# Kernel tuning notes

Measured on AMD Instinct MI355X. Metric: run time of the kernel, lower is better.

The kernel has to match this reference:

```python
import jax, jax.numpy as jnp
import numpy as np

B, N, M = 2, 256, 512
IN_F, OUT_F = 256, 128
NEG_INF = -1.0e12


def setup_inputs() -> dict:
    key = jax.random.key(0)
    kx, ka, kw, kv = jax.random.split(key, 4)
    X = jax.random.normal(kx, (B, N, IN_F), dtype=jnp.float32)
    # node-edge incidence (0/1), kept float as in the torch module
    A = jax.random.randint(ka, (B, N, M), 0, 2).astype(jnp.float32)
    # xavier-uniform-ish scale: gain*sqrt(6/(fan_in+fan_out))
    w_scale = 1.414 * np.sqrt(6.0 / (IN_F + OUT_F))
    a_scale = 1.414 * np.sqrt(6.0 / (2 * OUT_F + 1))
    W = jax.random.uniform(kw, (IN_F, OUT_F), jnp.float32, -w_scale, w_scale)
    a = jax.random.uniform(kv, (2 * OUT_F, 1), jnp.float32, -a_scale, a_scale)
    return {"X": X, "A": A, "W": W, "a": a}


def reference(X, A, W, a):
    H = X @ W                                   # [B, N, F]
    F_ = H.shape[-1]
    # per-edge degree, zeros clamped to 1
    degree = jnp.sum(A, axis=1)[..., None]      # [B, M, 1]
    degree = jnp.where(degree == 0, 1.0, degree)
    Em = jnp.einsum('bnm,bnf->bmf', A, H) / degree   # [B, M, F]
    # faithful replication of torch: cat along dim=1 then view (note: NOT a
    # per-pair concat along features; rows of H and Em get interleaved)
    Hrep = jnp.tile(H, (1, 1, M)).reshape(B, N * M, F_)   # [B, N*M, F]
    EmRep = jnp.tile(Em, (1, N, 1))                        # [B, N*M, F]
    a_input = jnp.concatenate([Hrep, EmRep], axis=1).reshape(B, N, M, 2 * F_)
    e = jax.nn.leaky_relu(jnp.squeeze(a_input @ a, -1), negative_slope=0.01)  # [B, N, M]
    attention = jax.nn.softmax(jnp.where(A > 0, e, NEG_INF), axis=2)          # [B, N, M]
    h_prime = jnp.einsum('bnm,bnf->bmf', attention, H)                         # [B, M, F]
    return h_prime
```

## Files before the change

### kernel.cpp

```cpp
#include <hip/hip_runtime.h>

#define NN 256
#define MM 512
#define INF_ 256
#define OUTF 128

__global__ __launch_bounds__(256) void k_gemm(const float* __restrict__ X,
                                              const float* __restrict__ W,
                                              const float* __restrict__ avec,
                                              float* __restrict__ H,
                                              float* __restrict__ h0,
                                              float* __restrict__ h1,
                                              float* __restrict__ cH,
                                              float* __restrict__ S) {
    const int blk = blockIdx.x;
    const int t = threadIdx.x;
    const int f = t & 127, kh = t >> 7;
    const int bn0 = blk * 2, bn1 = bn0 + 1;
    __shared__ float xs[2][INF_];
    xs[0][t] = X[bn0 * INF_ + t];
    xs[1][t] = X[bn1 * INF_ + t];
    __syncthreads();
    float acc0 = 0.f, acc1 = 0.f;
    const float* Wp = W + kh * 128 * OUTF + f;
    const float* x0 = xs[0] + kh * 128;
    const float* x1 = xs[1] + kh * 128;
#pragma unroll 8
    for (int k = 0; k < 128; ++k) {
        float w = Wp[k * OUTF];
        acc0 = fmaf(x0[k], w, acc0);
        acc1 = fmaf(x1[k], w, acc1);
    }
    __shared__ float accs[2][256];
    accs[0][t] = acc0;
    accs[1][t] = acc1;
    __syncthreads();
    const int r = t >> 7, tf = t & 127;
    const int bn = bn0 + r;
    float a2 = accs[r][tf] + accs[r][tf + 128];
    H[bn * OUTF + tf] = a2;
    float p0 = a2 * avec[tf];
    float p1 = a2 * avec[OUTF + tf];
#pragma unroll
    for (int off = 32; off >= 1; off >>= 1) {
        p0 += __shfl_down(p0, off);
        p1 += __shfl_down(p1, off);
    }
    __shared__ float r0[4], r1[4];
    const int wv = t >> 6, ln = t & 63;
    if (ln == 0) { r0[wv] = p0; r1[wv] = p1; }
    __syncthreads();
    if (ln == 0 && (wv & 1) == 0) {
        float s0 = r0[wv] + r0[wv + 1];
        float s1 = r1[wv] + r1[wv + 1];
        h0[bn] = s0;
        h1[bn] = s1;
        float hA = s0 + s1;
        cH[bn] = hA > 0.f ? hA : 0.01f * hA;
        int n = bn & 255;
        if (n >= 128) S[(bn >> 8) * 128 + n - 128] = 0.f;
    }
}

__global__ __launch_bounds__(256) void k_emg(const float* __restrict__ A,
                                             const float* __restrict__ h0,
                                             const float* __restrict__ h1,
                                             const float* __restrict__ cH,
                                             float* __restrict__ g,
                                             float* __restrict__ rs0,
                                             float* __restrict__ rs1,
                                             float* __restrict__ S) {
    const int blk = blockIdx.x;
    const int t = threadIdx.x;
    if (blk < 32) {
        const int b = blk >> 4, mq = blk & 15;
        const int m_l = t & 31, n_l = t >> 5;
        __shared__ float sh0[NN], sh1[NN];
        __shared__ float sd[256], ss0[256], ss1[256];
        __shared__ float se0[32], se1[32], sg[16];
        sh0[t] = h0[b * NN + t];
        sh1[t] = h1[b * NN + t];
        __syncthreads();
        const float* Ap = A + (size_t)b * NN * MM + mq * 32 + m_l;
        float d = 0.f, s0 = 0.f, s1 = 0.f;
#pragma unroll 8
        for (int i = 0; i < 32; ++i) {
            int n = n_l * 32 + i;
            float av = Ap[n * MM];
            d += av;
            s0 += av * sh0[n];
            s1 += av * sh1[n];
        }
        sd[t] = d; ss0[t] = s0; ss1[t] = s1;
        __syncthreads();
        if (t < 32) {
            float D = 0.f, S0 = 0.f, S1 = 0.f;
#pragma unroll
            for (int j = 0; j < 8; ++j) {
                D  += sd[j * 32 + t];
                S0 += ss0[j * 32 + t];
                S1 += ss1[j * 32 + t];
            }
            if (D == 0.f) D = 1.f;
            se0[t] = S0 / D;
            se1[t] = S1 / D;
        }
        __syncthreads();
        if (t < 16) {
            float v = se0[2 * t] + se1[2 * t + 1];
            v = v > 0.f ? v : 0.01f * v;
            float gv = expf(v);
            g[b * MM + 16 * mq + t] = gv;
            g[b * MM + 256 + 16 * mq + t] = gv;
            sg[t] = gv;
        }
        __syncthreads();
        {
            const int u = t & 15, ng = t >> 4;
            const float gv = sg[u];
            const float* Alo = A + (size_t)b * NN * MM + 16 * mq + u;
#pragma unroll
            for (int step = 0; step < 8; ++step) {
                int n = 128 + ng + 16 * step;
                const float* Ar = Alo + (size_t)n * MM;
                float val = gv * (Ar[0] + Ar[256]);
                val += __shfl_xor(val, 1);
                val += __shfl_xor(val, 2);
                val += __shfl_xor(val, 4);
                val += __shfl_xor(val, 8);
                if (u == 0) atomicAdd(&S[b * 128 + n - 128], val);
            }
        }
    } else {
        const int wv = t >> 6, lane = t & 63;
        const int l = (blk - 32) * 4 + wv;
        const int b = l >> 7, n = l & 127;
        const int bn = b * NN + n;
        const float* Ar = A + (size_t)bn * MM;
        float c0 = 0.f, c1 = 0.f;
#pragma unroll
        for (int i = 0; i < 8; ++i) {
            float av = Ar[lane + 64 * i];
            if (i < 4) c0 += av; else c1 += av;
        }
#pragma unroll
        for (int off = 32; off >= 1; off >>= 1) {
            c0 += __shfl_xor(c0, off);
            c1 += __shfl_xor(c1, off);
        }
        if (lane == 0) {
            float ch0 = cH[b * NN + 2 * n];
            float ch1 = cH[b * NN + 2 * n + 1];
            float mx = fmaxf(c0 > 0.f ? ch0 : -INFINITY,
                             c1 > 0.f ? ch1 : -INFINITY);
            float e0 = c0 > 0.f ? expf(ch0 - mx) : 0.f;
            float e1 = c1 > 0.f ? expf(ch1 - mx) : 0.f;
            float inv = 1.f / (c0 * e0 + c1 * e1);
            rs0[bn] = e0 * inv;
            rs1[bn] = e1 * inv;
        }
    }
}

__global__ __launch_bounds__(256) void k_out(const float* __restrict__ A,
                                             const float* __restrict__ H,
                                             const float* __restrict__ g,
                                             const float* __restrict__ rs0,
                                             const float* __restrict__ rs1,
                                             const float* __restrict__ S,
                                             float* __restrict__ out) {
    __shared__ float sW[NN];
    __shared__ float sA[4][NN];
    __shared__ float2 sacc[2][4][64];
    const int blk = blockIdx.x;
    const int b = blk >> 7, mq = blk & 127;
    const int m_base = 4 * mq;
    const int t = threadIdx.x;
    if (t < 128) {
        sW[t] = ((mq < 64) ? rs0 : rs1)[b * NN + t];
    } else {
        sW[t] = 1.f / S[b * 128 + (t - 128)];
    }
    const float* Ac = A + (size_t)(b * NN + t) * MM + m_base;
    sA[0][t] = Ac[0];
    sA[1][t] = Ac[1];
    sA[2][t] = Ac[2];
    sA[3][t] = Ac[3];
    __syncthreads();
    const int f2 = t & 63;
    const int nh = (t >> 6) & 1;
    const int mh = t >> 7;
    const float* sA0 = sA[2 * mh];
    const float* sA1 = sA[2 * mh + 1];
    const float2* H2 = (const float2*)H + (size_t)b * NN * 64 + f2;
    float2 acc0 = {0.f, 0.f}, acc1 = {0.f, 0.f};
#pragma unroll 8
    for (int i = 0; i < 128; ++i) {
        int n = nh * 128 + i;
        float w = sW[n];
        float2 hv = H2[n * 64];
        float c0 = sA0[n] * w;
        float c1 = sA1[n] * w;
        acc0.x = fmaf(c0, hv.x, acc0.x);
        acc0.y = fmaf(c0, hv.y, acc0.y);
        acc1.x = fmaf(c1, hv.x, acc1.x);
        acc1.y = fmaf(c1, hv.y, acc1.y);
    }
    sacc[nh][2 * mh][f2] = acc0;
    sacc[nh][2 * mh + 1][f2] = acc1;
    __syncthreads();
    {
        const int ml = t >> 6, f2b = t & 63;
        const int m = m_base + ml;
        float eE = g[b * MM + m];
        float2 lo = sacc[0][ml][f2b];
        float2 hi = sacc[1][ml][f2b];
        float2 r;
        r.x = lo.x + eE * hi.x;
        r.y = lo.y + eE * hi.y;
        ((float2*)out)[((size_t)b * MM + m) * 64 + f2b] = r;
    }
}

extern "C" void kernel_launch(void* const* d_in, const int* in_sizes, int n_in,
                              void* d_out, int out_size, void* d_ws, size_t ws_size,
                              hipStream_t stream) {
    const float* X = (const float*)d_in[0];
    const float* A = (const float*)d_in[1];
    const float* W = (const float*)d_in[2];
    const float* a = (const float*)d_in[3];
    float* out = (float*)d_out;
    float* ws = (float*)d_ws;

    float* H   = ws;
    float* h0  = ws + 65536;
    float* h1  = ws + 66048;
    float* cH  = ws + 66560;
    float* g   = ws + 67072;
    float* rs0 = ws + 68096;
    float* rs1 = ws + 68608;
    float* S   = ws + 69120;

    k_gemm<<<256, 256, 0, stream>>>(X, W, a, H, h0, h1, cH, S);
    k_emg<<<96, 256, 0, stream>>>(A, h0, h1, cH, g, rs0, rs1, S);
    k_out<<<256, 256, 0, stream>>>(A, H, g, rs0, rs1, S, out);
}
```

Baseline: 24.65 us.

## Move softmax row normalization into GEMM kernel and widen per-block tiles

The per-node row count and softmax normalization (rs0/rs1), previously computed by extra blocks in the edge kernel, are now computed inside the GEMM kernel. Each GEMM block handles four nodes and also reads the matching A rows. That removes the cH round trip and shrinks the edge kernel to 32 blocks. The GEMM and output kernels now process 4 rows and 8 edges per block respectively, and the output kernel loads A with float4. This raises reuse of W and H per block but halves the grid size, which reduces parallelism on a wide GPU.

Result: slower. 29.73 us (+20.6%).

```diff
diff --git a/kernel.cpp b/kernel.cpp
--- a/kernel.cpp
+++ b/kernel.cpp
@@ -6,158 +6,174 @@
 #define OUTF 128
 
 __global__ __launch_bounds__(256) void k_gemm(const float* __restrict__ X,
+                                              const float* __restrict__ A,
                                               const float* __restrict__ W,
                                               const float* __restrict__ avec,
                                               float* __restrict__ H,
                                               float* __restrict__ h0,
                                               float* __restrict__ h1,
-                                              float* __restrict__ cH,
+                                              float* __restrict__ rs0,
+                                              float* __restrict__ rs1,
                                               float* __restrict__ S) {
     const int blk = blockIdx.x;
+    const int b = blk >> 6, q = blk & 63;
+    const int bn0 = b * NN + 4 * q;
     const int t = threadIdx.x;
     const int f = t & 127, kh = t >> 7;
-    const int bn0 = blk * 2, bn1 = bn0 + 1;
-    __shared__ float xs[2][INF_];
-    xs[0][t] = X[bn0 * INF_ + t];
-    xs[1][t] = X[bn1 * INF_ + t];
-    __syncthreads();
-    float acc0 = 0.f, acc1 = 0.f;
-    const float* Wp = W + kh * 128 * OUTF + f;
-    const float* x0 = xs[0] + kh * 128;
-    const float* x1 = xs[1] + kh * 128;
+    const int wv = t >> 6, ln = t & 63;
+
+    __shared__ float xs[4][INF_];
+    __shared__ float accs[4][256];
+    __shared__ float r0[4], r1[4];
+    __shared__ float sch[4];
+    __shared__ float scnt[4];
+
+    xs[0][t] = X[(bn0 + 0) * INF_ + t];
+    xs[1][t] = X[(bn0 + 1) * INF_ + t];
+    xs[2][t] = X[(bn0 + 2) * INF_ + t];
+    xs[3][t] = X[(bn0 + 3) * INF_ + t];
+    __syncthreads();
+
+    float acc0 = 0.f, acc1 = 0.f, acc2 = 0.f, acc3 = 0.f;
+    {
+        const float* Wp = W + kh * 128 * OUTF + f;
+        const float* x0 = xs[0] + kh * 128;
+        const float* x1 = xs[1] + kh * 128;
+        const float* x2 = xs[2] + kh * 128;
+        const float* x3 = xs[3] + kh * 128;
 #pragma unroll 8
-    for (int k = 0; k < 128; ++k) {
-        float w = Wp[k * OUTF];
-        acc0 = fmaf(x0[k], w, acc0);
-        acc1 = fmaf(x1[k], w, acc1);
-    }
-    __shared__ float accs[2][256];
+        for (int k = 0; k < 128; ++k) {
+            float w = Wp[k * OUTF];
+            acc0 = fmaf(x0[k], w, acc0);
+            acc1 = fmaf(x1[k], w, acc1);
+            acc2 = fmaf(x2[k], w, acc2);
+            acc3 = fmaf(x3[k], w, acc3);
+        }
+    }
     accs[0][t] = acc0;
     accs[1][t] = acc1;
-    __syncthreads();
-    const int r = t >> 7, tf = t & 127;
-    const int bn = bn0 + r;
-    float a2 = accs[r][tf] + accs[r][tf + 128];
-    H[bn * OUTF + tf] = a2;
-    float p0 = a2 * avec[tf];
-    float p1 = a2 * avec[OUTF + tf];
-#pragma unroll
-    for (int off = 32; off >= 1; off >>= 1) {
-        p0 += __shfl_down(p0, off);
-        p1 += __shfl_down(p1, off);
-    }
-    __shared__ float r0[4], r1[4];
-    const int wv = t >> 6, ln = t & 63;
-    if (ln == 0) { r0[wv] = p0; r1[wv] = p1; }
-    __syncthreads();
-    if (ln == 0 && (wv & 1) == 0) {
-        float s0 = r0[wv] + r0[wv + 1];
-        float s1 = r1[wv] + r1[wv + 1];
-        h0[bn] = s0;
-        h1[bn] = s1;
-        float hA = s0 + s1;
-        cH[bn] = hA > 0.f ? hA : 0.01f * hA;
-        int n = bn & 255;
-        if (n >= 128) S[(bn >> 8) * 128 + n - 128] = 0.f;
-    }
-}
-
-__global__ __launch_bounds__(256) void k_emg(const float* __restrict__ A,
-                                             const float* __restrict__ h0,
-                                             const float* __restrict__ h1,
-                                             const float* __restrict__ cH,
-                                             float* __restrict__ g,
-                                             float* __restrict__ rs0,
-                                             float* __restrict__ rs1,
-                                             float* __restrict__ S) {
-    const int blk = blockIdx.x;
-    const int t = threadIdx.x;
-    if (blk < 32) {
-        const int b = blk >> 4, mq = blk & 15;
-        const int m_l = t & 31, n_l = t >> 5;
-        __shared__ float sh0[NN], sh1[NN];
-        __shared__ float sd[256], ss0[256], ss1[256];
-        __shared__ float se0[32], se1[32], sg[16];
-        sh0[t] = h0[b * NN + t];
-        sh1[t] = h1[b * NN + t];
+    accs[2][t] = acc2;
+    accs[3][t] = acc3;
+    __syncthreads();
+
+#pragma unroll
+    for (int pass = 0; pass < 2; ++pass) {
+        const int row = 2 * pass + (t >> 7);
+        const int tf = t & 127;
+        float a2 = accs[row][tf] + accs[row][tf + 128];
+        H[(bn0 + row) * OUTF + tf] = a2;
+        float p0 = a2 * avec[tf];
+        float p1 = a2 * avec[OUTF + tf];
+#pragma unroll
+        for (int off = 32; off >= 1; off >>= 1) {
+            p0 += __shfl_down(p0, off);
+            p1 += __shfl_down(p1, off);
+        }
+        if (ln == 0) { r0[wv] = p0; r1[wv] = p1; }
         __syncthreads();
-        const float* Ap = A + (size_t)b * NN * MM + mq * 32 + m_l;
-        float d = 0.f, s0 = 0.f, s1 = 0.f;
-#pragma unroll 8
-        for (int i = 0; i < 32; ++i) {
-            int n = n_l * 32 + i;
-            float av = Ap[n * MM];
-            d += av;
-            s0 += av * sh0[n];
-            s1 += av * sh1[n];
-        }
-        sd[t] = d; ss0[t] = s0; ss1[t] = s1;
+        if (ln == 0 && (wv & 1) == 0) {
+            const int r = 2 * pass + (wv >> 1);
+            float s0 = r0[wv] + r0[wv + 1];
+            float s1 = r1[wv] + r1[wv + 1];
+            h0[bn0 + r] = s0;
+            h1[bn0 + r] = s1;
+            float hA = s0 + s1;
+            sch[r] = hA > 0.f ? hA : 0.01f * hA;
+        }
         __syncthreads();
-        if (t < 32) {
-            float D = 0.f, S0 = 0.f, S1 = 0.f;
-#pragma unroll
-            for (int j = 0; j < 8; ++j) {
-                D  += sd[j * 32 + t];
-                S0 += ss0[j * 32 + t];
-                S1 += ss1[j * 32 + t];
-            }
-            if (D == 0.f) D = 1.f;
-            se0[t] = S0 / D;
-            se1[t] = S1 / D;
-        }
+    }
+
+    {
+        const int sr = wv >> 1, half = wv & 1;
+        const int n = 2 * q + sr;
+        const float* Ar = A + (size_t)(b * NN + n) * MM + half * 256;
+        float c = 0.f;
+#pragma unroll
+        for (int i = 0; i < 4; ++i) c += Ar[ln + 64 * i];
+#pragma unroll
+        for (int off = 32; off >= 1; off >>= 1) c += __shfl_xor(c, off);
+        if (ln == 0) scnt[wv] = c;
         __syncthreads();
-        if (t < 16) {
-            float v = se0[2 * t] + se1[2 * t + 1];
-            v = v > 0.f ? v : 0.01f * v;
-            float gv = expf(v);
-            g[b * MM + 16 * mq + t] = gv;
-            g[b * MM + 256 + 16 * mq + t] = gv;
-            sg[t] = gv;
-        }
-        __syncthreads();
-        {
-            const int u = t & 15, ng = t >> 4;
-            const float gv = sg[u];
-            const float* Alo = A + (size_t)b * NN * MM + 16 * mq + u;
-#pragma unroll
-            for (int step = 0; step < 8; ++step) {
-                int n = 128 + ng + 16 * step;
-                const float* Ar = Alo + (size_t)n * MM;
-                float val = gv * (Ar[0] + Ar[256]);
-                val += __shfl_xor(val, 1);
-                val += __shfl_xor(val, 2);
-                val += __shfl_xor(val, 4);
-                val += __shfl_xor(val, 8);
-                if (u == 0) atomicAdd(&S[b * 128 + n - 128], val);
-            }
-        }
-    } else {
-        const int wv = t >> 6, lane = t & 63;
-        const int l = (blk - 32) * 4 + wv;
-        const int b = l >> 7, n = l & 127;
-        const int bn = b * NN + n;
-        const float* Ar = A + (size_t)bn * MM;
-        float c0 = 0.f, c1 = 0.f;
-#pragma unroll
-        for (int i = 0; i < 8; ++i) {
-            float av = Ar[lane + 64 * i];
-            if (i < 4) c0 += av; else c1 += av;
-        }
-#pragma unroll
-        for (int off = 32; off >= 1; off >>= 1) {
-            c0 += __shfl_xor(c0, off);
-            c1 += __shfl_xor(c1, off);
-        }
-        if (lane == 0) {
-            float ch0 = cH[b * NN + 2 * n];
-            float ch1 = cH[b * NN + 2 * n + 1];
+        if (t < 2) {
+            const int j = t;
+            float c0 = scnt[2 * j], c1 = scnt[2 * j + 1];
+            float ch0 = sch[2 * j], ch1 = sch[2 * j + 1];
             float mx = fmaxf(c0 > 0.f ? ch0 : -INFINITY,
                              c1 > 0.f ? ch1 : -INFINITY);
             float e0 = c0 > 0.f ? expf(ch0 - mx) : 0.f;
             float e1 = c1 > 0.f ? expf(ch1 - mx) : 0.f;
             float inv = 1.f / (c0 * e0 + c1 * e1);
+            const int bn = b * NN + 2 * q + j;
             rs0[bn] = e0 * inv;
             rs1[bn] = e1 * inv;
+            S[b * 128 + 2 * q + j] = 0.f;
+        }
+    }
+}
+
+__global__ __launch_bounds__(256) void k_emg(const float* __restrict__ A,
+                                             const float* __restrict__ h0,
+                                             const float* __restrict__ h1,
+                                             float* __restrict__ g,
+                                             float* __restrict__ S) {
+    const int blk = blockIdx.x;
+    const int t = threadIdx.x;
+    const int b = blk >> 4, mq = blk & 15;
+    const int m_l = t & 31, n_l = t >> 5;
+    __shared__ float sh0[NN], sh1[NN];
+    __shared__ float sd[256], ss0[256], ss1[256];
+    __shared__ float se0[32], se1[32], sg[16];
+    sh0[t] = h0[b * NN + t];
+    sh1[t] = h1[b * NN + t];
+    __syncthreads();
+    const float* Ap = A + (size_t)b * NN * MM + mq * 32 + m_l;
+    float d = 0.f, s0 = 0.f, s1 = 0.f;
+#pragma unroll 8
+    for (int i = 0; i < 32; ++i) {
+        int n = n_l * 32 + i;
+        float av = Ap[n * MM];
+        d += av;
+        s0 += av * sh0[n];
+        s1 += av * sh1[n];
+    }
+    sd[t] = d; ss0[t] = s0; ss1[t] = s1;
+    __syncthreads();
+    if (t < 32) {
+        float D = 0.f, S0 = 0.f, S1 = 0.f;
+#pragma unroll
+        for (int j = 0; j < 8; ++j) {
+            D  += sd[j * 32 + t];
+            S0 += ss0[j * 32 + t];
+            S1 += ss1[j * 32 + t];
+        }
+        if (D == 0.f) D = 1.f;
+        se0[t] = S0 / D;
+        se1[t] = S1 / D;
+    }
+    __syncthreads();
+    if (t < 16) {
+        float v = se0[2 * t] + se1[2 * t + 1];
+        v = v > 0.f ? v : 0.01f * v;
+        float gv = expf(v);
+        g[b * MM + 16 * mq + t] = gv;
+        g[b * MM + 256 + 16 * mq + t] = gv;
+        sg[t] = gv;
+    }
+    __syncthreads();
+    {
+        const int u = t & 15, ng = t >> 4;
+        const float gv = sg[u];
+        const float* Alo = A + (size_t)b * NN * MM + 16 * mq + u;
+#pragma unroll
+        for (int step = 0; step < 8; ++step) {
+            int n = 128 + ng + 16 * step;
+            const float* Ar = Alo + (size_t)n * MM;
+            float val = gv * (Ar[0] + Ar[256]);
+            val += __shfl_xor(val, 1);
+            val += __shfl_xor(val, 2);
+            val += __shfl_xor(val, 4);
+            val += __shfl_xor(val, 8);
+            if (u == 0) atomicAdd(&S[b * 128 + n - 128], val);
         }
     }
 }
@@ -170,30 +186,34 @@
                                              const float* __restrict__ S,
                                              float* __restrict__ out) {
     __shared__ float sW[NN];
-    __shared__ float sA[4][NN];
-    __shared__ float2 sacc[2][4][64];
+    __shared__ float sA[8][NN];
+    __shared__ float2 sacc[2][8][64];
     const int blk = blockIdx.x;
-    const int b = blk >> 7, mq = blk & 127;
-    const int m_base = 4 * mq;
+    const int b = blk >> 6, mo = blk & 63;
+    const int m_base = 8 * mo;
     const int t = threadIdx.x;
     if (t < 128) {
-        sW[t] = ((mq < 64) ? rs0 : rs1)[b * NN + t];
+        sW[t] = ((mo < 32) ? rs0 : rs1)[b * NN + t];
     } else {
         sW[t] = 1.f / S[b * 128 + (t - 128)];
     }
-    const float* Ac = A + (size_t)(b * NN + t) * MM + m_base;
-    sA[0][t] = Ac[0];
-    sA[1][t] = Ac[1];
-    sA[2][t] = Ac[2];
-    sA[3][t] = Ac[3];
+    {
+        const float4* Ar = (const float4*)(A + (size_t)(b * NN + t) * MM + m_base);
+        float4 a0 = Ar[0], a1 = Ar[1];
+        sA[0][t] = a0.x; sA[1][t] = a0.y; sA[2][t] = a0.z; sA[3][t] = a0.w;
+        sA[4][t] = a1.x; sA[5][t] = a1.y; sA[6][t] = a1.z; sA[7][t] = a1.w;
+    }
     __syncthreads();
     const int f2 = t & 63;
     const int nh = (t >> 6) & 1;
-    const int mh = t >> 7;
-    const float* sA0 = sA[2 * mh];
-    const float* sA1 = sA[2 * mh + 1];
+    const int mg = t >> 7;
+    const float* sA0 = sA[4 * mg];
+    const float* sA1 = sA[4 * mg + 1];
+    const float* sA2 = sA[4 * mg + 2];
+    const float* sA3 = sA[4 * mg + 3];
     const float2* H2 = (const float2*)H + (size_t)b * NN * 64 + f2;
-    float2 acc0 = {0.f, 0.f}, acc1 = {0.f, 0.f};
+    float2 accA = {0.f, 0.f}, accB = {0.f, 0.f};
+    float2 accC = {0.f, 0.f}, accD = {0.f, 0.f};
 #pragma unroll 8
     for (int i = 0; i < 128; ++i) {
         int n = nh * 128 + i;
@@ -201,24 +221,32 @@
         float2 hv = H2[n * 64];
         float c0 = sA0[n] * w;
         float c1 = sA1[n] * w;
-        acc0.x = fmaf(c0, hv.x, acc0.x);
-        acc0.y = fmaf(c0, hv.y, acc0.y);
-        acc1.x = fmaf(c1, hv.x, acc1.x);
-        acc1.y = fmaf(c1, hv.y, acc1.y);
-    }
-    sacc[nh][2 * mh][f2] = acc0;
-    sacc[nh][2 * mh + 1][f2] = acc1;
-    __syncthreads();
-    {
-        const int ml = t >> 6, f2b = t & 63;
+        float c2 = sA2[n] * w;
+        float c3 = sA3[n] * w;
+        accA.x = fmaf(c0, hv.x, accA.x); accA.y = fmaf(c0, hv.y, accA.y);
+        accB.x = fmaf(c1, hv.x, accB.x); accB.y = fmaf(c1, hv.y, accB.y);
+        accC.x = fmaf(c2, hv.x, accC.x); accC.y = fmaf(c2, hv.y, accC.y);
+        accD.x = fmaf(c3, hv.x, accD.x); accD.y = fmaf(c3, hv.y, accD.y);
+    }
+    sacc[nh][4 * mg + 0][f2] = accA;
+    sacc[nh][4 * mg + 1][f2] = accB;
+    sacc[nh][4 * mg + 2][f2] = accC;
+    sacc[nh][4 * mg + 3][f2] = accD;
+    __syncthreads();
+    {
+        const int ml = t >> 5, f2b = t & 31;
         const int m = m_base + ml;
-        float eE = g[b * MM + m];
-        float2 lo = sacc[0][ml][f2b];
-        float2 hi = sacc[1][ml][f2b];
-        float2 r;
-        r.x = lo.x + eE * hi.x;
-        r.y = lo.y + eE * hi.y;
-        ((float2*)out)[((size_t)b * MM + m) * 64 + f2b] = r;
+        const float eE = g[b * MM + m];
+#pragma unroll
+        for (int s = 0; s < 2; ++s) {
+            const int fx = f2b + 32 * s;
+            float2 lo = sacc[0][ml][fx];
+            float2 hi = sacc[1][ml][fx];
+            float2 r;
+            r.x = lo.x + eE * hi.x;
+            r.y = lo.y + eE * hi.y;
+            ((float2*)out)[((size_t)b * MM + m) * 64 + fx] = r;
+        }
     }
 }
 
@@ -235,13 +263,12 @@
     float* H   = ws;
     float* h0  = ws + 65536;
     float* h1  = ws + 66048;
-    float* cH  = ws + 66560;
-    float* g   = ws + 67072;
-    float* rs0 = ws + 68096;
-    float* rs1 = ws + 68608;
-    float* S   = ws + 69120;
-
-    k_gemm<<<256, 256, 0, stream>>>(X, W, a, H, h0, h1, cH, S);
-    k_emg<<<96, 256, 0, stream>>>(A, h0, h1, cH, g, rs0, rs1, S);
-    k_out<<<256, 256, 0, stream>>>(A, H, g, rs0, rs1, S, out);
-}
+    float* g   = ws + 66560;
+    float* rs0 = ws + 67584;
+    float* rs1 = ws + 68096;
+    float* S   = ws + 68608;
+
+    k_gemm<<<128, 256, 0, stream>>>(X, A, W, a, H, h0, h1, rs0, rs1, S);
+    k_emg<<<32, 256, 0, stream>>>(A, h0, h1, g, S);
+    k_out<<<128, 256, 0, stream>>>(A, H, g, rs0, rs1, S, out);
+}
```

## Vectorize GEMM and output kernels with float4 loads and split-K reductions

Applied to the files above, without the earlier changes.

The projection kernel now has each thread load float4 slices of W and accumulate 4 output features over a 32-wide K chunk, then reduces 8 partials in shared memory. The output kernel has each thread compute 4 edges by 4 features from float4 H loads over 32 nodes, with an 8-way shared-memory reduction. Both changes aim to raise arithmetic per global load and cut load instruction count, at the cost of more registers and a larger shared-memory reduction with fewer active threads in the final phase.

Result: faster. 23.89 us (-3.1%).

```diff
diff --git a/kernel.cpp b/kernel.cpp
--- a/kernel.cpp
+++ b/kernel.cpp
@@ -15,50 +15,58 @@
                                               float* __restrict__ S) {
     const int blk = blockIdx.x;
     const int t = threadIdx.x;
-    const int f = t & 127, kh = t >> 7;
-    const int bn0 = blk * 2, bn1 = bn0 + 1;
+    const int bn0 = blk * 2;
     __shared__ float xs[2][INF_];
+    __shared__ float4 sacc[2][8][32];
     xs[0][t] = X[bn0 * INF_ + t];
-    xs[1][t] = X[bn1 * INF_ + t];
-    __syncthreads();
-    float acc0 = 0.f, acc1 = 0.f;
-    const float* Wp = W + kh * 128 * OUTF + f;
-    const float* x0 = xs[0] + kh * 128;
-    const float* x1 = xs[1] + kh * 128;
+    xs[1][t] = X[(bn0 + 1) * INF_ + t];
+    __syncthreads();
+
+    const int f4 = t & 31, kg = t >> 5;
+    const float4* W4 = (const float4*)W;
+    float4 acc0 = {0.f, 0.f, 0.f, 0.f}, acc1 = {0.f, 0.f, 0.f, 0.f};
+    const int k0 = kg * 32;
 #pragma unroll 8
-    for (int k = 0; k < 128; ++k) {
-        float w = Wp[k * OUTF];
-        acc0 = fmaf(x0[k], w, acc0);
-        acc1 = fmaf(x1[k], w, acc1);
-    }
-    __shared__ float accs[2][256];
-    accs[0][t] = acc0;
-    accs[1][t] = acc1;
-    __syncthreads();
-    const int r = t >> 7, tf = t & 127;
-    const int bn = bn0 + r;
-    float a2 = accs[r][tf] + accs[r][tf + 128];
-    H[bn * OUTF + tf] = a2;
-    float p0 = a2 * avec[tf];
-    float p1 = a2 * avec[OUTF + tf];
-#pragma unroll
-    for (int off = 32; off >= 1; off >>= 1) {
-        p0 += __shfl_down(p0, off);
-        p1 += __shfl_down(p1, off);
-    }
-    __shared__ float r0[4], r1[4];
-    const int wv = t >> 6, ln = t & 63;
-    if (ln == 0) { r0[wv] = p0; r1[wv] = p1; }
-    __syncthreads();
-    if (ln == 0 && (wv & 1) == 0) {
-        float s0 = r0[wv] + r0[wv + 1];
-        float s1 = r1[wv] + r1[wv + 1];
-        h0[bn] = s0;
-        h1[bn] = s1;
-        float hA = s0 + s1;
-        cH[bn] = hA > 0.f ? hA : 0.01f * hA;
-        int n = bn & 255;
-        if (n >= 128) S[(bn >> 8) * 128 + n - 128] = 0.f;
+    for (int i = 0; i < 32; ++i) {
+        const int k = k0 + i;
+        float4 w = W4[k * 32 + f4];
+        float x0v = xs[0][k], x1v = xs[1][k];
+        acc0.x = fmaf(x0v, w.x, acc0.x); acc0.y = fmaf(x0v, w.y, acc0.y);
+        acc0.z = fmaf(x0v, w.z, acc0.z); acc0.w = fmaf(x0v, w.w, acc0.w);
+        acc1.x = fmaf(x1v, w.x, acc1.x); acc1.y = fmaf(x1v, w.y, acc1.y);
+        acc1.z = fmaf(x1v, w.z, acc1.z); acc1.w = fmaf(x1v, w.w, acc1.w);
+    }
+    sacc[0][kg][f4] = acc0;
+    sacc[1][kg][f4] = acc1;
+    __syncthreads();
+
+    if (t < 64) {
+        const int r = t >> 5, fb = t & 31;
+        float4 s = {0.f, 0.f, 0.f, 0.f};
+#pragma unroll
+        for (int j = 0; j < 8; ++j) {
+            float4 v = sacc[r][j][fb];
+            s.x += v.x; s.y += v.y; s.z += v.z; s.w += v.w;
+        }
+        ((float4*)H)[(bn0 + r) * 32 + fb] = s;
+        const float4* av4 = (const float4*)avec;
+        float4 a0 = av4[fb], a1 = av4[32 + fb];
+        float p0 = s.x*a0.x + s.y*a0.y + s.z*a0.z + s.w*a0.w;
+        float p1 = s.x*a1.x + s.y*a1.y + s.z*a1.z + s.w*a1.w;
+#pragma unroll
+        for (int off = 16; off >= 1; off >>= 1) {
+            p0 += __shfl_xor(p0, off);
+            p1 += __shfl_xor(p1, off);
+        }
+        if ((t & 31) == 0) {
+            const int bn = bn0 + r;
+            h0[bn] = p0;
+            h1[bn] = p1;
+            float hA = p0 + p1;
+            cH[bn] = hA > 0.f ? hA : 0.01f * hA;
+            const int n = bn & 255;
+            if (n >= 128) S[(bn >> 8) * 128 + n - 128] = 0.f;
+        }
     }
 }
 
@@ -171,7 +179,7 @@
                                              float* __restrict__ out) {
     __shared__ float sW[NN];
     __shared__ float sA[4][NN];
-    __shared__ float2 sacc[2][4][64];
+    __shared__ float4 sacc[8][4][32];
     const int blk = blockIdx.x;
     const int b = blk >> 7, mq = blk & 127;
     const int m_base = 4 * mq;
@@ -181,44 +189,58 @@
     } else {
         sW[t] = 1.f / S[b * 128 + (t - 128)];
     }
-    const float* Ac = A + (size_t)(b * NN + t) * MM + m_base;
-    sA[0][t] = Ac[0];
-    sA[1][t] = Ac[1];
-    sA[2][t] = Ac[2];
-    sA[3][t] = Ac[3];
-    __syncthreads();
-    const int f2 = t & 63;
-    const int nh = (t >> 6) & 1;
-    const int mh = t >> 7;
-    const float* sA0 = sA[2 * mh];
-    const float* sA1 = sA[2 * mh + 1];
-    const float2* H2 = (const float2*)H + (size_t)b * NN * 64 + f2;
-    float2 acc0 = {0.f, 0.f}, acc1 = {0.f, 0.f};
+    {
+        const float4* Ar = (const float4*)(A + (size_t)(b * NN + t) * MM + m_base);
+        float4 a = Ar[0];
+        sA[0][t] = a.x; sA[1][t] = a.y; sA[2][t] = a.z; sA[3][t] = a.w;
+    }
+    __syncthreads();
+    const int f4 = t & 31, ng = t >> 5;
+    const float4* H4 = (const float4*)H + (size_t)b * NN * 32 + f4;
+    float4 A0 = {0.f,0.f,0.f,0.f}, A1 = {0.f,0.f,0.f,0.f};
+    float4 A2 = {0.f,0.f,0.f,0.f}, A3 = {0.f,0.f,0.f,0.f};
+    const int n0 = ng * 32;
 #pragma unroll 8
-    for (int i = 0; i < 128; ++i) {
-        int n = nh * 128 + i;
+    for (int i = 0; i < 32; ++i) {
+        const int n = n0 + i;
         float w = sW[n];
-        float2 hv = H2[n * 64];
-        float c0 = sA0[n] * w;
-        float c1 = sA1[n] * w;
-        acc0.x = fmaf(c0, hv.x, acc0.x);
-        acc0.y = fmaf(c0, hv.y, acc0.y);
-        acc1.x = fmaf(c1, hv.x, acc1.x);
-        acc1.y = fmaf(c1, hv.y, acc1.y);
-    }
-    sacc[nh][2 * mh][f2] = acc0;
-    sacc[nh][2 * mh + 1][f2] = acc1;
-    __syncthreads();
-    {
-        const int ml = t >> 6, f2b = t & 63;
+        float4 hv = H4[n * 32];
+        float c0 = sA[0][n] * w;
+        float c1 = sA[1][n] * w;
+        float c2 = sA[2][n] * w;
+        float c3 = sA[3][n] * w;
+        A0.x = fmaf(c0, hv.x, A0.x); A0.y = fmaf(c0, hv.y, A0.y);
+        A0.z = fmaf(c0, hv.z, A0.z); A0.w = fmaf(c0, hv.w, A0.w);
+        A1.x = fmaf(c1, hv.x, A1.x); A1.y = fmaf(c1, hv.y, A1.y);
+        A1.z = fmaf(c1, hv.z, A1.z); A1.w = fmaf(c1, hv.w, A1.w);
+        A2.x = fmaf(c2, hv.x, A2.x); A2.y = fmaf(c2, hv.y, A2.y);
+        A2.z = fmaf(c2, hv.z, A2.z); A2.w = fmaf(c2, hv.w, A2.w);
+        A3.x = fmaf(c3, hv.x, A3.x); A3.y = fmaf(c3, hv.y, A3.y);
+        A3.z = fmaf(c3, hv.z, A3.z); A3.w = fmaf(c3, hv.w, A3.w);
+    }
+    sacc[ng][0][f4] = A0;
+    sacc[ng][1][f4] = A1;
+    sacc[ng][2][f4] = A2;
+    sacc[ng][3][f4] = A3;
+    __syncthreads();
+    if (t < 128) {
+        const int ml = t >> 5, fb = t & 31;
+        float4 lo = {0.f,0.f,0.f,0.f}, hi = {0.f,0.f,0.f,0.f};
+#pragma unroll
+        for (int j = 0; j < 4; ++j) {
+            float4 vl = sacc[j][ml][fb];
+            float4 vh = sacc[4 + j][ml][fb];
+            lo.x += vl.x; lo.y += vl.y; lo.z += vl.z; lo.w += vl.w;
+            hi.x += vh.x; hi.y += vh.y; hi.z += vh.z; hi.w += vh.w;
+        }
         const int m = m_base + ml;
-        float eE = g[b * MM + m];
-        float2 lo = sacc[0][ml][f2b];
-        float2 hi = sacc[1][ml][f2b];
-        float2 r;
+        const float eE = g[b * MM + m];
+        float4 r;
         r.x = lo.x + eE * hi.x;
         r.y = lo.y + eE * hi.y;
-        ((float2*)out)[((size_t)b * MM + m) * 64 + f2b] = r;
+        r.z = lo.z + eE * hi.z;
+        r.w = lo.w + eE * hi.w;
+        ((float4*)out)[((size_t)b * MM + m) * 32 + fb] = r;
     }
 }
 
```
